# Optimization experiments

Measured on AMD Instinct MI355X. Metric: run time of the kernel, lower is better.

The kernel has to match this reference:

```python
import jax, jax.numpy as jnp
import numpy as np

D = 768
H0, H1 = 1536, 768  # mlp_layers '1536,768'


def setup_inputs() -> dict:
    key = jax.random.key(0)
    ks = jax.random.split(key, 8)
    bsz, C, l_x, l_y = 8, 64, 256, 256
    xs = jax.random.normal(ks[0], (bsz, l_x, D), dtype=jnp.float32)
    ys = jax.random.normal(ks[1], (bsz, C, l_y, D), dtype=jnp.float32)
    # torch.nn.Linear weights: [out_features, in_features]
    def lin(k, fout, fin):
        bound = 1.0 / np.sqrt(fin)
        kw, kb = jax.random.split(k)
        W = jax.random.uniform(kw, (fout, fin), jnp.float32, -bound, bound)
        b = jax.random.uniform(kb, (fout,), jnp.float32, -bound, bound)
        return W, b
    W0, b0 = lin(ks[2], H0, 2 * D)
    W1, b1 = lin(ks[3], H1, H0)
    W2, b2 = lin(ks[4], 1, H1)
    return {"xs": xs, "ys": ys, "W0": W0, "b0": b0, "W1": W1, "b1": b1, "W2": W2, "b2": b2}


def reference(xs, ys, W0, b0, W1, b1, W2, b2):
    bsz, l_x, d = xs.shape
    _, C, l_y, _ = ys.shape
    # dot-product scores: [bsz, C, l_x, l_y]
    scores = jnp.einsum('bxd,bcyd->bcxy', xs, ys)
    argmax_idx = jnp.argmax(scores, axis=-1)  # [bsz, C, l_x]
    # gather winning y vector for each x token: [bsz, C, l_x, d]
    idx = jnp.broadcast_to(argmax_idx[..., None], (bsz, C, l_x, d))
    y_sel = jnp.take_along_axis(ys, idx, axis=2)
    xs_exp = jnp.broadcast_to(xs[:, None], (bsz, C, l_x, d))
    # stack then flatten(start_dim=-2) == concat along last dim: [bsz,C,l_x,2d]
    h = jnp.concatenate([xs_exp, y_sel], axis=-1)
    # MLP (dropout is identity at inference)
    h = jax.nn.softplus(jnp.einsum('bcxi,oi->bcxo', h, W0) + b0)
    h = jax.nn.softplus(jnp.einsum('bcxi,oi->bcxo', h, W1) + b1)
    s = jnp.einsum('bcxi,oi->bcxo', h, W2) + b2  # [bsz,C,l_x,1]
    return jnp.sum(s[..., 0], axis=-1)  # [bsz, C]
```

## Files before the change

### kernel.cpp

```cpp
#include <hip/hip_runtime.h>
#include <stdint.h>

#define DB   8
#define DC   64
#define DLX  256
#define DLY  256
#define DD   768
#define DH0  1536
#define DH1  768
#define NBC  (DB*DC)
#define NTOK (NBC*DLX)
#define TAU  0.25f

typedef float f32x4 __attribute__((ext_vector_type(4)));
typedef _Float16 f16x8 __attribute__((ext_vector_type(8)));
typedef _Float16 f16x4 __attribute__((ext_vector_type(4)));

__device__ __forceinline__ float softplusf(float x){
  float t = __builtin_amdgcn_exp2f(-fabsf(x) * 1.44269504f);
  return fmaxf(x, 0.0f) + 0.69314718f * __builtin_amdgcn_logf(1.0f + t);
}

__device__ __forceinline__ void gload_lds16(const void* g, void* l){
  __builtin_amdgcn_global_load_lds((const __attribute__((address_space(1))) void*)g,
                                   (__attribute__((address_space(3))) void*)l,
                                   16, 0, 0);
}

__global__ __launch_bounds__(256) void k_cvt16(const float* __restrict__ src, int ld, int off,
                                               int rows, int cols, _Float16* __restrict__ dst){
  int total = rows * (cols >> 3);
  for (int idx = blockIdx.x * 256 + threadIdx.x; idx < total; idx += gridDim.x * 256){
    int r = idx / (cols >> 3), c8 = (idx % (cols >> 3)) * 8;
    const float* s = src + (size_t)r * ld + off + c8;
    float4 f0 = *(const float4*)s, f1 = *(const float4*)(s + 4);
    f16x8 v;
    v[0]=(_Float16)f0.x; v[1]=(_Float16)f0.y; v[2]=(_Float16)f0.z; v[3]=(_Float16)f0.w;
    v[4]=(_Float16)f1.x; v[5]=(_Float16)f1.y; v[6]=(_Float16)f1.z; v[7]=(_Float16)f1.w;
    *(f16x8*)(dst + (size_t)r * cols + c8) = v;
  }
}

__global__ __launch_bounds__(1024, 1) void k_scores3(const _Float16* __restrict__ xs16,
                                                     const _Float16* __restrict__ ys16,
                                                     const float* __restrict__ xs,
                                                     const float* __restrict__ ys,
                                                     int* __restrict__ widx){
  const int bc = blockIdx.y, b = bc >> 6;
  const int x0 = blockIdx.x * 128;
  const float* X = xs + ((size_t)b * DLX + x0) * DD;
  const float* Y = ys + (size_t)bc * DLY * DD;
  __shared__ __align__(16) _Float16 As[128 * 32];
  __shared__ __align__(16) _Float16 Bs[256 * 32];
  __shared__ float rmx[128][4];
  __shared__ float gm[128];
  __shared__ unsigned short cand[128][8];
  __shared__ int ccnt[128];
  const int tid = threadIdx.x;
  const int l = tid & 63, w = tid >> 6;
  const int wr = w >> 2, wc = w & 3;
  const int lrow = l & 15, lg = l >> 4;
  const int kq = (lg ^ (lrow & 3)) * 8;
  const int srow = l >> 2;
  const int kg = (((l & 3) ^ ((l >> 2) & 3))) * 8;
  const _Float16* srcB = ys16 + ((size_t)bc * DLY + w*16 + srow) * DD + kg;
  const _Float16* srcA = xs16 + ((size_t)b * DLX + x0 + (w & 7)*16 + srow) * DD + kg;

  f32x4 acc[2][4];
  #pragma unroll
  for (int i = 0; i < 2; i++)
    #pragma unroll
    for (int j = 0; j < 4; j++) acc[i][j] = (f32x4){0.f,0.f,0.f,0.f};

  for (int k0 = 0; k0 < DD; k0 += 32){
    __syncthreads();
    gload_lds16(srcB + k0, Bs + w*512);
    if (w < 8) gload_lds16(srcA + k0, As + w*512);
    __syncthreads();
    f16x8 af[2], bf[4];
    #pragma unroll
    for (int i = 0; i < 2; i++)
      af[i] = *(const f16x8*)&As[(wr*32 + i*16 + lrow)*32 + kq];
    #pragma unroll
    for (int j = 0; j < 4; j++)
      bf[j] = *(const f16x8*)&Bs[(wc*64 + j*16 + lrow)*32 + kq];
    #pragma unroll
    for (int i = 0; i < 2; i++)
      #pragma unroll
      for (int j = 0; j < 4; j++)
        acc[i][j] = __builtin_amdgcn_mfma_f32_16x16x32_f16(af[i], bf[j], acc[i][j], 0, 0, 0);
  }

  #pragma unroll
  for (int i = 0; i < 2; i++)
    #pragma unroll
    for (int r = 0; r < 4; r++){
      float m = fmaxf(fmaxf(acc[i][0][r], acc[i][1][r]), fmaxf(acc[i][2][r], acc[i][3][r]));
      m = fmaxf(m, __shfl_xor(m, 1));
      m = fmaxf(m, __shfl_xor(m, 2));
      m = fmaxf(m, __shfl_xor(m, 4));
      m = fmaxf(m, __shfl_xor(m, 8));
      if (lrow == 0) rmx[wr*32 + i*16 + lg*4 + r][wc] = m;
    }
  __syncthreads();
  if (tid < 128){
    gm[tid] = fmaxf(fmaxf(rmx[tid][0], rmx[tid][1]), fmaxf(rmx[tid][2], rmx[tid][3]));
    ccnt[tid] = 0;
  }
  __syncthreads();
  #pragma unroll
  for (int i = 0; i < 2; i++)
    #pragma unroll
    for (int r = 0; r < 4; r++){
      int t = wr*32 + i*16 + lg*4 + r;
      float thr = gm[t] - TAU;
      #pragma unroll
      for (int j = 0; j < 4; j++){
        float s = acc[i][j][r];
        if (s >= thr){
          int p = atomicAdd(&ccnt[t], 1);
          if (p < 8) cand[t][p] = (unsigned short)(wc*64 + j*16 + lrow);
        }
      }
    }
  __syncthreads();
  for (int it = 0; it < 8; it++){
    int t = w * 8 + it;
    int cnt = ccnt[t];
    int by;
    if (cnt == 1){
      by = cand[t][0];
    } else {
      const float* xr = X + (size_t)t * DD;
      float best = -1e30f; int besty = 0;
      int n = (cnt <= 8) ? cnt : 256;
      for (int p = 0; p < n; p++){
        int c = (cnt <= 8) ? (int)cand[t][p] : p;
        const float* yr = Y + (size_t)c * DD;
        float s = 0.f;
        #pragma unroll
        for (int q = 0; q < 3; q++){
          float4 xv = *(const float4*)(xr + l*12 + q*4);
          float4 yv = *(const float4*)(yr + l*12 + q*4);
          s += xv.x*yv.x + xv.y*yv.y + xv.z*yv.z + xv.w*yv.w;
        }
        s += __shfl_xor(s, 1);  s += __shfl_xor(s, 2);  s += __shfl_xor(s, 4);
        s += __shfl_xor(s, 8);  s += __shfl_xor(s, 16); s += __shfl_xor(s, 32);
        if (s > best || (s == best && c < besty)){ best = s; besty = c; }
      }
      by = besty;
    }
    if (l == 0) widx[(size_t)bc * DLX + x0 + t] = by;
  }
}

template<int MODE>
__global__ __launch_bounds__(512) void k_gemm16(const _Float16* __restrict__ A,
        const _Float16* __restrict__ B,
        const int* __restrict__ widx,
        const _Float16* __restrict__ X0h,
        const float* __restrict__ bias,
        const float* __restrict__ w2,
        float* __restrict__ outF,
        _Float16* __restrict__ outH){
  constexpr int K = (MODE == 2) ? DH0 : DD;
  __shared__ __align__(16) _Float16 As[128 * 32];
  __shared__ __align__(16) _Float16 Bs[256 * 32];
  const int tid = threadIdx.x;
  const int gx = gridDim.x, nwg = gx * gridDim.y;
  int lin = blockIdx.x + gx * blockIdx.y;
  int swz = (lin & 7) * (nwg >> 3) + (lin >> 3);
  const int n0  = (swz % gx) * 256;
  const int by  = swz / gx;
  const int rt0 = by * 128;
  const int l = tid & 63, w = tid >> 6;
  const int wr = w >> 2, wc = w & 3;
  const int lrow = l & 15, lg = l >> 4;
  const int kq = (lg ^ (lrow & 3)) * 8;
  const int kg = (((l & 3) ^ ((l >> 2) & 3))) * 8;

  int bc = 0, xb = 0, b = 0;
  if constexpr (MODE == 1){ bc = by >> 1; xb = (by & 1) * 128; b = bc >> 6; }

  const _Float16* gsrc[3];
  _Float16* ldst[3];
  #pragma unroll
  for (int i = 0; i < 3; i++){
    int u = w*3 + i;
    if (u < 8){
      int row = u*16 + (l >> 2);
      if constexpr (MODE == 1){
        int yi = widx[bc * DLX + xb + row];
        gsrc[i] = A + ((size_t)bc * DLY + yi) * DD + kg;
      } else {
        gsrc[i] = A + (size_t)(rt0 + row) * K + kg;
      }
      ldst[i] = (_Float16*)As + u*512;
    } else {
      int row = (u - 8)*16 + (l >> 2);
      gsrc[i] = B + (size_t)(n0 + row) * K + kg;
      ldst[i] = (_Float16*)Bs + (u - 8)*512;
    }
  }

  f32x4 acc[4][4];
  #pragma unroll
  for (int i = 0; i < 4; i++)
    #pragma unroll
    for (int j = 0; j < 4; j++) acc[i][j] = (f32x4){0.f,0.f,0.f,0.f};

  for (int k0 = 0; k0 < K; k0 += 32){
    __syncthreads();
    gload_lds16(gsrc[0] + k0, ldst[0]);
    gload_lds16(gsrc[1] + k0, ldst[1]);
    gload_lds16(gsrc[2] + k0, ldst[2]);
    __syncthreads();
    f16x8 af[4], bf[4];
    #pragma unroll
    for (int i = 0; i < 4; i++){
      af[i] = *(const f16x8*)&As[(wr*64 + i*16 + lrow)*32 + kq];
      bf[i] = *(const f16x8*)&Bs[(wc*64 + i*16 + lrow)*32 + kq];
    }
    #pragma unroll
    for (int i = 0; i < 4; i++)
      #pragma unroll
      for (int j = 0; j < 4; j++)
        acc[i][j] = __builtin_amdgcn_mfma_f32_16x16x32_f16(af[i], bf[j], acc[i][j], 0, 0, 0);
  }

  if constexpr (MODE == 0){
    #pragma unroll
    for (int mi = 0; mi < 4; mi++)
      #pragma unroll
      for (int ni = 0; ni < 4; ni++){
        int n = n0 + wc*64 + ni*16 + lrow;
        float bv = bias[n];
        #pragma unroll
        for (int r = 0; r < 4; r++){
          int m = wr*64 + mi*16 + lg*4 + r;
          outH[(size_t)(rt0 + m) * DH0 + n] = (_Float16)(acc[mi][ni][r] + bv);
        }
      }
  } else if constexpr (MODE == 1){
    #pragma unroll
    for (int mi = 0; mi < 4; mi++)
      #pragma unroll
      for (int ni = 0; ni < 4; ni++){
        int n = n0 + wc*64 + ni*16 + lrow;
        #pragma unroll
        for (int r = 0; r < 4; r++){
          int m = wr*64 + mi*16 + lg*4 + r;
          float x0v = (float)X0h[((size_t)b * DLX + xb + m) * DH0 + n];
          float v = softplusf(acc[mi][ni][r] + x0v);
          outH[(size_t)(rt0 + m) * DH0 + n] = (_Float16)v;
        }
      }
  } else {
    float p[4][4];
    #pragma unroll
    for (int mi = 0; mi < 4; mi++)
      #pragma unroll
      for (int r = 0; r < 4; r++) p[mi][r] = 0.f;
    #pragma unroll
    for (int ni = 0; ni < 4; ni++){
      int n = n0 + wc*64 + ni*16 + lrow;
      float b1v = bias[n], w2v = w2[n];
      #pragma unroll
      for (int mi = 0; mi < 4; mi++)
        #pragma unroll
        for (int r = 0; r < 4; r++)
          p[mi][r] += softplusf(acc[mi][ni][r] + b1v) * w2v;
    }
    const int nb = (int)(swz % gx);
    #pragma unroll
    for (int mi = 0; mi < 4; mi++)
      #pragma unroll
      for (int r = 0; r < 4; r++){
        float s = p[mi][r];
        s += __shfl_xor(s, 1);
        s += __shfl_xor(s, 2);
        s += __shfl_xor(s, 4);
        s += __shfl_xor(s, 8);
        if (lrow == 0){
          size_t t = (size_t)rt0 + wr*64 + mi*16 + lg*4 + r;
          outF[t * 12 + nb*4 + wc] = s;
        }
      }
  }
}

__global__ __launch_bounds__(256) void k_reduce(const float* __restrict__ spart,
                                                const float* __restrict__ b2,
                                                float* __restrict__ out){
  int bc = blockIdx.x, tid = threadIdx.x;
  const float* p = spart + ((size_t)bc * DLX + tid) * 12;
  float s = 0.0f;
  #pragma unroll
  for (int j = 0; j < 12; j++) s += p[j];
  __shared__ float red[256];
  red[tid] = s;
  __syncthreads();
  for (int off = 128; off > 0; off >>= 1){
    if (tid < off) red[tid] += red[tid + off];
    __syncthreads();
  }
  if (tid == 0) out[bc] = red[0] + 256.0f * b2[0];
}

extern "C" void kernel_launch(void* const* d_in, const int* in_sizes, int n_in,
                              void* d_out, int out_size, void* d_ws, size_t ws_size,
                              hipStream_t stream){
  const float* xs = (const float*)d_in[0];
  const float* ys = (const float*)d_in[1];
  const float* W0 = (const float*)d_in[2];
  const float* b0 = (const float*)d_in[3];
  const float* W1 = (const float*)d_in[4];
  const float* b1 = (const float*)d_in[5];
  const float* W2 = (const float*)d_in[6];
  const float* b2 = (const float*)d_in[7];
  float* out = (float*)d_out;

  char* wsp = (char*)d_ws;
  size_t off = 0;
  auto alloc = [&](size_t bytes)->void*{
    void* p = wsp + off;
    off += (bytes + 255) & ~(size_t)255;
    return p;
  };
  int* widx        = (int*)alloc((size_t)NTOK * 4);
  _Float16* ys16   = (_Float16*)alloc((size_t)NBC * DLY * DD * 2);
  _Float16* xs16   = (_Float16*)alloc((size_t)DB * DLX * DD * 2);
  _Float16* W0xf   = (_Float16*)alloc((size_t)DH0 * DD * 2);
  _Float16* W0yf   = (_Float16*)alloc((size_t)DH0 * DD * 2);
  _Float16* W1f    = (_Float16*)alloc((size_t)DH1 * DH0 * 2);
  _Float16* X0h    = (_Float16*)alloc((size_t)DB * DLX * DH0 * 2);
  float* spart     = (float*)alloc((size_t)NTOK * 12 * 4);
  _Float16* H0     = (_Float16*)alloc((size_t)NTOK * DH0 * 2);

  k_cvt16<<<dim3(576),  256, 0, stream>>>(W0, DH0, 0,  DH0, DD, W0xf);
  k_cvt16<<<dim3(576),  256, 0, stream>>>(W0, DH0, DD, DH0, DD, W0yf);
  k_cvt16<<<dim3(576),  256, 0, stream>>>(W1, DH0, 0,  DH1, DH0, W1f);
  k_cvt16<<<dim3(768),  256, 0, stream>>>(xs, DD, 0, DB*DLX, DD, xs16);
  k_cvt16<<<dim3(4096), 256, 0, stream>>>(ys, DD, 0, NBC*DLY, DD, ys16);
  k_scores3<<<dim3(2, NBC), 1024, 0, stream>>>(xs16, ys16, xs, ys, widx);
  k_gemm16<0><<<dim3(6, 16),   512, 0, stream>>>(xs16, W0xf, nullptr, nullptr, b0, nullptr, nullptr, X0h);
  k_gemm16<1><<<dim3(6, 1024), 512, 0, stream>>>(ys16, W0yf, widx, X0h, nullptr, nullptr, nullptr, H0);
  k_gemm16<2><<<dim3(3, 1024), 512, 0, stream>>>(H0, W1f, nullptr, nullptr, b1, W2, spart, nullptr);
  k_reduce<<<NBC, 256, 0, stream>>>(spart, b2, out);
}
```

Before: 1.063 ms.

## Double-buffer LDS tiles in scores and GEMM kernels to overlap loads with MFMA

Both the scores kernel and the templated GEMM kernel now use two LDS buffers per operand. The next k-slice is issued with global_load_lds into the alternate buffer while MFMAs run on the current one, and the loop needs one barrier per iteration instead of two. This aims to hide global-to-LDS latency behind compute. LDS use doubles, which may reduce occupancy for the 512-thread GEMM. It also relies on the barrier covering completion of the async global_load_lds writes.

```diff
diff --git a/kernel.cpp b/kernel.cpp
--- a/kernel.cpp
+++ b/kernel.cpp
@@ -50,8 +50,8 @@
   const int x0 = blockIdx.x * 128;
   const float* X = xs + ((size_t)b * DLX + x0) * DD;
   const float* Y = ys + (size_t)bc * DLY * DD;
-  __shared__ __align__(16) _Float16 As[128 * 32];
-  __shared__ __align__(16) _Float16 Bs[256 * 32];
+  __shared__ __align__(16) _Float16 As[2][128 * 32];
+  __shared__ __align__(16) _Float16 Bs[2][256 * 32];
   __shared__ float rmx[128][4];
   __shared__ float gm[128];
   __shared__ unsigned short cand[128][8];
@@ -72,23 +72,30 @@
     #pragma unroll
     for (int j = 0; j < 4; j++) acc[i][j] = (f32x4){0.f,0.f,0.f,0.f};
 
+  gload_lds16(srcB, &Bs[0][w*512]);
+  if (w < 8) gload_lds16(srcA, &As[0][w*512]);
+  __syncthreads();
+
+  int cur = 0;
   for (int k0 = 0; k0 < DD; k0 += 32){
-    __syncthreads();
-    gload_lds16(srcB + k0, Bs + w*512);
-    if (w < 8) gload_lds16(srcA + k0, As + w*512);
-    __syncthreads();
+    if (k0 + 32 < DD){
+      gload_lds16(srcB + k0 + 32, &Bs[cur^1][w*512]);
+      if (w < 8) gload_lds16(srcA + k0 + 32, &As[cur^1][w*512]);
+    }
     f16x8 af[2], bf[4];
     #pragma unroll
     for (int i = 0; i < 2; i++)
-      af[i] = *(const f16x8*)&As[(wr*32 + i*16 + lrow)*32 + kq];
+      af[i] = *(const f16x8*)&As[cur][(wr*32 + i*16 + lrow)*32 + kq];
     #pragma unroll
     for (int j = 0; j < 4; j++)
-      bf[j] = *(const f16x8*)&Bs[(wc*64 + j*16 + lrow)*32 + kq];
+      bf[j] = *(const f16x8*)&Bs[cur][(wc*64 + j*16 + lrow)*32 + kq];
     #pragma unroll
     for (int i = 0; i < 2; i++)
       #pragma unroll
       for (int j = 0; j < 4; j++)
         acc[i][j] = __builtin_amdgcn_mfma_f32_16x16x32_f16(af[i], bf[j], acc[i][j], 0, 0, 0);
+    __syncthreads();
+    cur ^= 1;
   }
 
   #pragma unroll
@@ -164,8 +171,8 @@
         float* __restrict__ outF,
         _Float16* __restrict__ outH){
   constexpr int K = (MODE == 2) ? DH0 : DD;
-  __shared__ __align__(16) _Float16 As[128 * 32];
-  __shared__ __align__(16) _Float16 Bs[256 * 32];
+  __shared__ __align__(16) _Float16 As[2][128 * 32];
+  __shared__ __align__(16) _Float16 Bs[2][256 * 32];
   const int tid = threadIdx.x;
   const int gx = gridDim.x, nwg = gx * gridDim.y;
   int lin = blockIdx.x + gx * blockIdx.y;
@@ -183,7 +190,8 @@
   if constexpr (MODE == 1){ bc = by >> 1; xb = (by & 1) * 128; b = bc >> 6; }
 
   const _Float16* gsrc[3];
-  _Float16* ldst[3];
+  _Float16* ld0[3];
+  _Float16* ld1[3];
   #pragma unroll
   for (int i = 0; i < 3; i++){
     int u = w*3 + i;
@@ -195,11 +203,11 @@
       } else {
         gsrc[i] = A + (size_t)(rt0 + row) * K + kg;
       }
-      ldst[i] = (_Float16*)As + u*512;
+      ld0[i] = &As[0][u*512]; ld1[i] = &As[1][u*512];
     } else {
       int row = (u - 8)*16 + (l >> 2);
       gsrc[i] = B + (size_t)(n0 + row) * K + kg;
-      ldst[i] = (_Float16*)Bs + (u - 8)*512;
+      ld0[i] = &Bs[0][(u-8)*512]; ld1[i] = &Bs[1][(u-8)*512];
     }
   }
 
@@ -209,23 +217,32 @@
     #pragma unroll
     for (int j = 0; j < 4; j++) acc[i][j] = (f32x4){0.f,0.f,0.f,0.f};
 
+  #pragma unroll
+  for (int i = 0; i < 3; i++) gload_lds16(gsrc[i], ld0[i]);
+  __syncthreads();
+
+  int cur = 0;
   for (int k0 = 0; k0 < K; k0 += 32){
-    __syncthreads();
-    gload_lds16(gsrc[0] + k0, ldst[0]);
-    gload_lds16(gsrc[1] + k0, ldst[1]);
-    gload_lds16(gsrc[2] + k0, ldst[2]);
-    __syncthreads();
+    if (k0 + 32 < K){
+      #pragma unroll
+      for (int i = 0; i < 3; i++)
+        gload_lds16(gsrc[i] + k0 + 32, cur ? ld0[i] : ld1[i]);
+    }
+    const _Float16* Ab = As[cur];
+    const _Float16* Bb = Bs[cur];
     f16x8 af[4], bf[4];
     #pragma unroll
     for (int i = 0; i < 4; i++){
-      af[i] = *(const f16x8*)&As[(wr*64 + i*16 + lrow)*32 + kq];
-      bf[i] = *(const f16x8*)&Bs[(wc*64 + i*16 + lrow)*32 + kq];
+      af[i] = *(const f16x8*)&Ab[(wr*64 + i*16 + lrow)*32 + kq];
+      bf[i] = *(const f16x8*)&Bb[(wc*64 + i*16 + lrow)*32 + kq];
     }
     #pragma unroll
     for (int i = 0; i < 4; i++)
       #pragma unroll
       for (int j = 0; j < 4; j++)
         acc[i][j] = __builtin_amdgcn_mfma_f32_16x16x32_f16(af[i], bf[j], acc[i][j], 0, 0, 0);
+    __syncthreads();
+    cur ^= 1;
   }
 
   if constexpr (MODE == 0){
```

New measurement: 1.167 ms. +9.8%, slower.

## Double GEMM K-tile to 64 and address A/B via 32-bit offsets from one base

Applied to the files above, without the earlier changes.

The fp16 GEMM kernels now stage 64-wide K slices per barrier pair instead of 32, with a new 8-slot XOR swizzle, and run two MFMA sub-steps per tile, halving the number of syncthreads. Global addresses for both operands are computed as unsigned offsets from the A pointer (B passed as an element delta), with workspace buffers reordered so the deltas fit, to cut 64-bit address arithmetic and register use. This doubles LDS use per block, which may reduce occupancy, and relies on the offsets not overflowing 32 bits.

```diff
diff --git a/kernel.cpp b/kernel.cpp
--- a/kernel.cpp
+++ b/kernel.cpp
@@ -156,7 +156,7 @@
 
 template<int MODE>
 __global__ __launch_bounds__(512) void k_gemm16(const _Float16* __restrict__ A,
-        const _Float16* __restrict__ B,
+        unsigned bdelta,
         const int* __restrict__ widx,
         const _Float16* __restrict__ X0h,
         const float* __restrict__ bias,
@@ -164,8 +164,8 @@
         float* __restrict__ outF,
         _Float16* __restrict__ outH){
   constexpr int K = (MODE == 2) ? DH0 : DD;
-  __shared__ __align__(16) _Float16 As[128 * 32];
-  __shared__ __align__(16) _Float16 Bs[256 * 32];
+  __shared__ __align__(16) _Float16 As[128 * 64];
+  __shared__ __align__(16) _Float16 Bs[256 * 64];
   const int tid = threadIdx.x;
   const int gx = gridDim.x, nwg = gx * gridDim.y;
   int lin = blockIdx.x + gx * blockIdx.y;
@@ -176,30 +176,32 @@
   const int l = tid & 63, w = tid >> 6;
   const int wr = w >> 2, wc = w & 3;
   const int lrow = l & 15, lg = l >> 4;
-  const int kq = (lg ^ (lrow & 3)) * 8;
-  const int kg = (((l & 3) ^ ((l >> 2) & 3))) * 8;
 
   int bc = 0, xb = 0, b = 0;
   if constexpr (MODE == 1){ bc = by >> 1; xb = (by & 1) * 128; b = bc >> 6; }
 
-  const _Float16* gsrc[3];
-  _Float16* ldst[3];
-  #pragma unroll
-  for (int i = 0; i < 3; i++){
-    int u = w*3 + i;
-    if (u < 8){
-      int row = u*16 + (l >> 2);
+  const int urow = l >> 3;
+  const int uslot = (l & 7) ^ (urow & 7);
+  unsigned goff[6];
+  _Float16* ldst[6];
+  #pragma unroll
+  for (int i = 0; i < 6; i++){
+    int u = w*6 + i;
+    if (u < 16){
+      int row = u*8 + urow;
+      unsigned aoff;
       if constexpr (MODE == 1){
         int yi = widx[bc * DLX + xb + row];
-        gsrc[i] = A + ((size_t)bc * DLY + yi) * DD + kg;
+        aoff = (unsigned)((bc * DLY + yi) * DD);
       } else {
-        gsrc[i] = A + (size_t)(rt0 + row) * K + kg;
-      }
+        aoff = (unsigned)((rt0 + row) * K);
+      }
+      goff[i] = aoff + uslot*8;
       ldst[i] = (_Float16*)As + u*512;
     } else {
-      int row = (u - 8)*16 + (l >> 2);
-      gsrc[i] = B + (size_t)(n0 + row) * K + kg;
-      ldst[i] = (_Float16*)Bs + (u - 8)*512;
+      int row = (u - 16)*8 + urow;
+      goff[i] = bdelta + (unsigned)((n0 + row) * K) + uslot*8;
+      ldst[i] = (_Float16*)Bs + (u - 16)*512;
     }
   }
 
@@ -209,23 +211,27 @@
     #pragma unroll
     for (int j = 0; j < 4; j++) acc[i][j] = (f32x4){0.f,0.f,0.f,0.f};
 
-  for (int k0 = 0; k0 < K; k0 += 32){
-    __syncthreads();
-    gload_lds16(gsrc[0] + k0, ldst[0]);
-    gload_lds16(gsrc[1] + k0, ldst[1]);
-    gload_lds16(gsrc[2] + k0, ldst[2]);
-    __syncthreads();
-    f16x8 af[4], bf[4];
-    #pragma unroll
-    for (int i = 0; i < 4; i++){
-      af[i] = *(const f16x8*)&As[(wr*64 + i*16 + lrow)*32 + kq];
-      bf[i] = *(const f16x8*)&Bs[(wc*64 + i*16 + lrow)*32 + kq];
-    }
-    #pragma unroll
-    for (int i = 0; i < 4; i++)
-      #pragma unroll
-      for (int j = 0; j < 4; j++)
-        acc[i][j] = __builtin_amdgcn_mfma_f32_16x16x32_f16(af[i], bf[j], acc[i][j], 0, 0, 0);
+  for (int k0 = 0; k0 < K; k0 += 64){
+    __syncthreads();
+    #pragma unroll
+    for (int i = 0; i < 6; i++)
+      gload_lds16(A + (size_t)(goff[i] + (unsigned)k0), ldst[i]);
+    __syncthreads();
+    #pragma unroll
+    for (int kh = 0; kh < 2; kh++){
+      const int rc = ((kh*4 + lg) ^ (lrow & 7)) * 8;
+      f16x8 af[4], bf[4];
+      #pragma unroll
+      for (int i = 0; i < 4; i++){
+        af[i] = *(const f16x8*)&As[(wr*64 + i*16 + lrow)*64 + rc];
+        bf[i] = *(const f16x8*)&Bs[(wc*64 + i*16 + lrow)*64 + rc];
+      }
+      #pragma unroll
+      for (int i = 0; i < 4; i++)
+        #pragma unroll
+        for (int j = 0; j < 4; j++)
+          acc[i][j] = __builtin_amdgcn_mfma_f32_16x16x32_f16(af[i], bf[j], acc[i][j], 0, 0, 0);
+    }
   }
 
   if constexpr (MODE == 0){
@@ -329,13 +335,17 @@
   };
   int* widx        = (int*)alloc((size_t)NTOK * 4);
   _Float16* ys16   = (_Float16*)alloc((size_t)NBC * DLY * DD * 2);
+  _Float16* W0yf   = (_Float16*)alloc((size_t)DH0 * DD * 2);
   _Float16* xs16   = (_Float16*)alloc((size_t)DB * DLX * DD * 2);
   _Float16* W0xf   = (_Float16*)alloc((size_t)DH0 * DD * 2);
-  _Float16* W0yf   = (_Float16*)alloc((size_t)DH0 * DD * 2);
-  _Float16* W1f    = (_Float16*)alloc((size_t)DH1 * DH0 * 2);
   _Float16* X0h    = (_Float16*)alloc((size_t)DB * DLX * DH0 * 2);
   float* spart     = (float*)alloc((size_t)NTOK * 12 * 4);
   _Float16* H0     = (_Float16*)alloc((size_t)NTOK * DH0 * 2);
+  _Float16* W1f    = (_Float16*)alloc((size_t)DH1 * DH0 * 2);
+
+  unsigned d0 = (unsigned)(W0xf - xs16);
+  unsigned d1 = (unsigned)(W0yf - ys16);
+  unsigned d2 = (unsigned)(W1f - H0);
 
   k_cvt16<<<dim3(576),  256, 0, stream>>>(W0, DH0, 0,  DH0, DD, W0xf);
   k_cvt16<<<dim3(576),  256, 0, stream>>>(W0, DH0, DD, DH0, DD, W0yf);
@@ -343,8 +353,8 @@
   k_cvt16<<<dim3(768),  256, 0, stream>>>(xs, DD, 0, DB*DLX, DD, xs16);
   k_cvt16<<<dim3(4096), 256, 0, stream>>>(ys, DD, 0, NBC*DLY, DD, ys16);
   k_scores3<<<dim3(2, NBC), 1024, 0, stream>>>(xs16, ys16, xs, ys, widx);
-  k_gemm16<0><<<dim3(6, 16),   512, 0, stream>>>(xs16, W0xf, nullptr, nullptr, b0, nullptr, nullptr, X0h);
-  k_gemm16<1><<<dim3(6, 1024), 512, 0, stream>>>(ys16, W0yf, widx, X0h, nullptr, nullptr, nullptr, H0);
-  k_gemm16<2><<<dim3(3, 1024), 512, 0, stream>>>(H0, W1f, nullptr, nullptr, b1, W2, spart, nullptr);
+  k_gemm16<0><<<dim3(6, 16),   512, 0, stream>>>(xs16, d0, nullptr, nullptr, b0, nullptr, nullptr, X0h);
+  k_gemm16<1><<<dim3(6, 1024), 512, 0, stream>>>(ys16, d1, widx, X0h, nullptr, nullptr, nullptr, H0);
+  k_gemm16<2><<<dim3(3, 1024), 512, 0, stream>>>(H0, d2, nullptr, nullptr, b1, W2, spart, nullptr);
   k_reduce<<<NBC, 256, 0, stream>>>(spart, b2, out);
 }
```

Result: faster. 990.6 us (-6.8%).
